# Kernel optimization log

Hardware: AMD Instinct MI355X
Metric: run time of the kernel (lower is better)

## Reference

```python
import jax, jax.numpy as jnp
import numpy as np

B, T, D, U = 64, 128, 1024, 1024


def setup_inputs() -> dict:
    key = jax.random.key(0)
    k_x, k_r, k_s, k_wi, k_wh = jax.random.split(key, 5)
    x = jax.random.normal(k_x, (B, T, D), dtype=jnp.float32)
    reset = jax.random.randint(k_r, (B, T), 0, 2, dtype=jnp.int32)
    state = jax.random.normal(k_s, (B, T, U), dtype=jnp.float32)
    # hk.GRU params: w_i (input->3*hidden), w_h (hidden->3*hidden), bias (3*hidden)
    w_i = jax.random.normal(k_wi, (D, 3 * U), dtype=jnp.float32) * (1.0 / np.sqrt(D))
    w_h = jax.random.normal(k_wh, (U, 3 * U), dtype=jnp.float32) * (1.0 / np.sqrt(U))
    b = jnp.zeros((3 * U,), dtype=jnp.float32)
    return {"x": x, "reset": reset, "state": state, "w_i": w_i, "w_h": w_h, "b": b}


def reference(x, reset, state, w_i, w_h, b):
    # _prepare_for_rnn merges (B,T)->rows and adds a length-1 time axis, so
    # hk.dynamic_unroll(ResetCore(GRU)) == one ResetCore(GRU) step over B*T rows.
    Bd, Td, Dd = x.shape
    Ud = w_h.shape[0]
    xf = x.reshape(Bd * Td, Dd)                      # [N, D]
    h = state.reshape(Bd * Td, Ud)                   # [N, U]
    should_reset = reset.reshape(Bd * Td, 1).astype(bool)
    # hk.ResetCore: replace state with initial_state (zeros) where reset is set
    h = jnp.where(should_reset, jnp.zeros_like(h), h)
    # hk.GRU step
    gates_x = xf @ w_i                               # [N, 3U]
    zr_x, a_x = gates_x[:, : 2 * Ud], gates_x[:, 2 * Ud :]
    zr = jax.nn.sigmoid(zr_x + h @ w_h[:, : 2 * Ud] + b[: 2 * Ud])
    z, r = zr[:, :Ud], zr[:, Ud:]
    a = jnp.tanh(a_x + (r * h) @ w_h[:, 2 * Ud :] + b[2 * Ud :])
    h_new = (1.0 - z) * h + z * a                    # [N, U]
    out = h_new.reshape(Bd, Td, Ud)                  # _recover_shape
    new_state = h_new.reshape(Bd, Td, Ud)            # _rnn_reshape back to (B,T,U)
    return out, new_state
```

## Files before the change

kernel.cpp:

```cpp
#include <hip/hip_runtime.h>


typedef __attribute__((ext_vector_type(8))) short short8;
typedef __attribute__((ext_vector_type(4))) short short4v;
typedef __attribute__((ext_vector_type(4))) float floatx4;
typedef __attribute__((ext_vector_type(4))) float f32x4;

#define MROWS 8192
#define KTOT 2048
#define NU 1024

__device__ __forceinline__ short f2bf(float f) {
  unsigned u = __builtin_bit_cast(unsigned, f);
  u += 0x7fffu + ((u >> 16) & 1u);
  return (short)(u >> 16);
}
__device__ __forceinline__ float bf2f(short s) {
  unsigned u = ((unsigned)(unsigned short)s) << 16;
  return __builtin_bit_cast(float, u);
}
__device__ __forceinline__ float sigmoid_f(float v) { return 1.f / (1.f + __expf(-v)); }
__device__ __forceinline__ float tanh_f(float v) {
  float c = fminf(fmaxf(v, -15.f), 15.f);
  float e = __expf(2.f * c);
  return (e - 1.f) / (e + 1.f);
}

typedef __attribute__((address_space(3))) void* lds_vp;
typedef const __attribute__((address_space(1))) void* gbl_vp;
__device__ __forceinline__ void gload16(const void* g, void* lds) {
  __builtin_amdgcn_global_load_lds((gbl_vp)g, (lds_vp)lds, 16, 0, 0);
}

__global__ __launch_bounds__(256) void wt_kernel(const float* __restrict__ w_i,
                                                 const float* __restrict__ w_h,
                                                 short* __restrict__ Wc) {
  __shared__ float tile[32][33];
  const int kb = blockIdx.x * 32;
  const int nb = blockIdx.y * 32;
  const float* src = (kb < 1024) ? w_i : w_h;
  const int kbl = kb & 1023;
  const int tx = threadIdx.x & 31;
  const int ty = threadIdx.x >> 5;
#pragma unroll
  for (int r = 0; r < 32; r += 8)
    tile[ty + r][tx] = src[(size_t)(kbl + ty + r) * 3072 + nb + tx];
  __syncthreads();
#pragma unroll
  for (int r = 0; r < 32; r += 8)
    Wc[(size_t)(nb + ty + r) * KTOT + kb + tx] = f2bf(tile[tx][ty + r]);
}

__global__ __launch_bounds__(256) void xh_kernel(const float* __restrict__ x,
                                                 const int* __restrict__ reset,
                                                 const float* __restrict__ state,
                                                 short* __restrict__ xbf,
                                                 short* __restrict__ hbf) {
  const size_t i4 = (size_t)blockIdx.x * blockDim.x + threadIdx.x;
  const size_t off = i4 * 4;
  const int row = (int)(off >> 10);
  const float hm = reset[row] ? 0.f : 1.f;
  floatx4 fx = *(const floatx4*)(x + off);
  floatx4 fh = *(const floatx4*)(state + off);
  short4v cx, ch;
#pragma unroll
  for (int e = 0; e < 4; ++e) { cx[e] = f2bf(fx[e]); ch[e] = f2bf(fh[e] * hm); }
  *(short4v*)(xbf + off) = cx;
  *(short4v*)(hbf + off) = ch;
}

struct TilePtrs {
  const short* a0; const short* a1;
  const short* h0; const short* h1;
  const short* b0; const short* b1;
};

#define GEMM_CORE(KHALF_SWITCH)                                              \
  f32x4 acc[4][4];                                                           \
  _Pragma("unroll") for (int i = 0; i < 4; ++i)                              \
      _Pragma("unroll") for (int j = 0; j < 4; ++j)                          \
          acc[i][j] = (f32x4){0.f, 0.f, 0.f, 0.f};                           \
  const int wave = tid >> 6, lane = tid & 63;                                \
  const int wm = wave >> 1, wn = wave & 1;                                   \
  const int lrow = lane & 15, lk = (lane >> 4) * 8;                          \
  char* ldsA0 = (char*)sA + wave * 1024; char* ldsA1 = ldsA0 + 4096;         \
  char* ldsB0 = (char*)sB + wave * 1024; char* ldsB1 = ldsB0 + 4096;         \
  for (int kk = 0; kk < KTOT; kk += 32) {                                    \
    const int kl = kk & 1023;                                                \
    const short *pa0, *pa1;                                                  \
    KHALF_SWITCH                                                             \
    gload16(pa0, ldsA0);                                                     \
    gload16(pa1, ldsA1);                                                     \
    gload16(p.b0 + kk, ldsB0);                                               \
    gload16(p.b1 + kk, ldsB1);                                               \
    __syncthreads();                                                         \
    short8 af[4], bfr[4];                                                    \
    _Pragma("unroll") for (int i = 0; i < 4; ++i)                            \
        af[i] = *(const short8*)&sA[wm * 64 + i * 16 + lrow][lk];            \
    _Pragma("unroll") for (int j = 0; j < 4; ++j)                            \
        bfr[j] = *(const short8*)&sB[wn * 64 + j * 16 + lrow][lk];           \
    _Pragma("unroll") for (int i = 0; i < 4; ++i)                            \
        _Pragma("unroll") for (int j = 0; j < 4; ++j)                        \
            acc[i][j] = __builtin_amdgcn_mfma_f32_16x16x32_bf16(             \
                af[i], bfr[j], acc[i][j], 0, 0, 0);                          \
    __syncthreads();                                                         \
  }

#define KSWITCH_STD                                                          \
  if (kk < 1024) { pa0 = p.a0 + kl; pa1 = p.a1 + kl; }                       \
  else           { pa0 = p.h0 + kl; pa1 = p.h1 + kl; }

__global__ __launch_bounds__(256, 3) void zr_kernel(
    const short* __restrict__ xbf, const short* __restrict__ hbf,
    const short* __restrict__ Wc, const float* __restrict__ bias,
    float* __restrict__ zbuf, short* __restrict__ rh) {
  __shared__ short sA[128][32];
  __shared__ short sB[128][32];
  const int tid = threadIdx.x;
  const int widx = (blockIdx.x & 7) * 128 + (blockIdx.x >> 3);
  const int m0 = (widx >> 4) * 128;
  const int n0 = (widx & 15) * 128;

  const int r0 = tid >> 2;
  const int kc = (tid & 3) * 8;
  TilePtrs p;
  p.a0 = xbf + (size_t)(m0 + r0) * 1024 + kc;
  p.a1 = xbf + (size_t)(m0 + 64 + r0) * 1024 + kc;
  p.h0 = hbf + (size_t)(m0 + r0) * 1024 + kc;
  p.h1 = hbf + (size_t)(m0 + 64 + r0) * 1024 + kc;
  p.b0 = Wc + (size_t)(n0 + r0) * KTOT + kc;
  p.b1 = Wc + (size_t)(n0 + 64 + r0) * KTOT + kc;

  GEMM_CORE(KSWITCH_STD)

  const bool zhalf = (n0 < 1024);
#pragma unroll
  for (int j = 0; j < 4; ++j) {
    const int gcn = n0 + wn * 64 + j * 16 + lrow;
    const float bv = bias[gcn];
#pragma unroll
    for (int i = 0; i < 4; ++i) {
#pragma unroll
      for (int rg = 0; rg < 4; ++rg) {
        const int gr = m0 + wm * 64 + i * 16 + (lane >> 4) * 4 + rg;
        const float sv = sigmoid_f(acc[i][j][rg] + bv);
        if (zhalf) {
          zbuf[(size_t)gr * NU + gcn] = sv;
        } else {
          const int u = gcn - 1024;
          const float hv = bf2f(hbf[(size_t)gr * NU + u]);
          rh[(size_t)gr * NU + u] = f2bf(sv * hv);
        }
      }
    }
  }
}

__global__ __launch_bounds__(256, 3) void cand_kernel(
    const short* __restrict__ xbf, const short* __restrict__ rh,
    const short* __restrict__ Wc, const float* __restrict__ bias,
    const int* __restrict__ reset, const float* __restrict__ state,
    const float* __restrict__ zbuf, float* __restrict__ out) {
  __shared__ short sA[128][32];
  __shared__ short sB[128][32];
  const int tid = threadIdx.x;
  const int widx = (blockIdx.x & 7) * 64 + (blockIdx.x >> 3);
  const int m0 = (widx >> 3) * 128;
  const int n0 = (widx & 7) * 128;

  const int r0 = tid >> 2;
  const int kc = (tid & 3) * 8;
  const short* Wa = Wc + (size_t)2048 * KTOT;
  TilePtrs p;
  p.a0 = xbf + (size_t)(m0 + r0) * 1024 + kc;
  p.a1 = xbf + (size_t)(m0 + 64 + r0) * 1024 + kc;
  p.h0 = rh + (size_t)(m0 + r0) * 1024 + kc;
  p.h1 = rh + (size_t)(m0 + 64 + r0) * 1024 + kc;
  p.b0 = Wa + (size_t)(n0 + r0) * KTOT + kc;
  p.b1 = Wa + (size_t)(n0 + 64 + r0) * KTOT + kc;

  GEMM_CORE(KSWITCH_STD)

#pragma unroll
  for (int j = 0; j < 4; ++j) {
    const int gc = n0 + wn * 64 + j * 16 + lrow;
    const float ba = bias[2048 + gc];
#pragma unroll
    for (int i = 0; i < 4; ++i) {
#pragma unroll
      for (int rg = 0; rg < 4; ++rg) {
        const int gr = m0 + wm * 64 + i * 16 + (lane >> 4) * 4 + rg;
        const float av = tanh_f(acc[i][j][rg] + ba);
        const float zv = zbuf[(size_t)gr * NU + gc];
        const float hv = reset[gr] ? 0.f : state[(size_t)gr * NU + gc];
        const float hn = (1.f - zv) * hv + zv * av;
        out[(size_t)gr * NU + gc] = hn;
        out[(size_t)MROWS * NU + (size_t)gr * NU + gc] = hn;
      }
    }
  }
}

extern "C" void kernel_launch(void* const* d_in, const int* in_sizes, int n_in,
                              void* d_out, int out_size, void* d_ws, size_t ws_size,
                              hipStream_t stream) {
  const float* x = (const float*)d_in[0];
  const int* reset = (const int*)d_in[1];
  const float* state = (const float*)d_in[2];
  const float* w_i = (const float*)d_in[3];
  const float* w_h = (const float*)d_in[4];
  const float* bias = (const float*)d_in[5];
  float* out = (float*)d_out;

  short* Wc = (short*)d_ws;
  short* xbf = Wc + (size_t)3072 * KTOT;
  short* hbf = xbf + (size_t)MROWS * 1024;
  short* rh  = hbf + (size_t)MROWS * 1024;
  float* zbuf = out + (size_t)MROWS * NU;

  wt_kernel<<<dim3(KTOT / 32, 3072 / 32), 256, 0, stream>>>(w_i, w_h, Wc);
  xh_kernel<<<dim3(MROWS * 1024 / 4 / 256), 256, 0, stream>>>(x, reset, state, xbf, hbf);

  zr_kernel<<<dim3(64 * 16), 256, 0, stream>>>(xbf, hbf, Wc, bias, zbuf, rh);
  cand_kernel<<<dim3(64 * 8), 256, 0, stream>>>(xbf, rh, Wc, bias, reset, state, zbuf, out);
}
```

Measured before the change: 196.7 us.

## Rewrite GEMM kernels with triple-buffered async LDS pipeline and 128x256 tiles

Both GEMM kernels are restructured to use 512-thread blocks with 128x256 output tiles and K-step 64. They also use a three-stage dynamic-LDS ring fed by global_load_lds with vmcnt-based waits, XOR-swizzled LDS addressing, and s_setprio around MFMA bursts. The x and masked-state bf16 copies are now written into one concatenated [N,2048] buffer so the A operand is a single contiguous row. This targets the load-then-barrier stalls and small-tile reuse of the previous single-buffered loop, at the cost of a large LDS footprint (one block per CU) and hand-managed wait counts that must stay correct.

```diff
diff --git a/kernel.cpp b/kernel.cpp
--- a/kernel.cpp
+++ b/kernel.cpp
@@ -9,6 +9,10 @@
 #define MROWS 8192
 #define KTOT 2048
 #define NU 1024
+#define NTILE 32
+#define ABYTES 16384
+#define BUFBYTES 49152
+#define LDSTOT (3 * BUFBYTES)
 
 __device__ __forceinline__ short f2bf(float f) {
   unsigned u = __builtin_bit_cast(unsigned, f);
@@ -31,6 +35,14 @@
 __device__ __forceinline__ void gload16(const void* g, void* lds) {
   __builtin_amdgcn_global_load_lds((gbl_vp)g, (lds_vp)lds, 16, 0, 0);
 }
+
+#define MF(a, b, c) __builtin_amdgcn_mfma_f32_16x16x32_bf16(a, b, c, 0, 0, 0)
+#define VMCNT(n) asm volatile("s_waitcnt vmcnt(" #n ")" ::: "memory")
+#define TILE_BAR()                          \
+  do {                                      \
+    __builtin_amdgcn_s_barrier();           \
+    asm volatile("" ::: "memory");          \
+  } while (0)
 
 __global__ __launch_bounds__(256) void wt_kernel(const float* __restrict__ w_i,
                                                  const float* __restrict__ w_h,
@@ -54,89 +66,136 @@
 __global__ __launch_bounds__(256) void xh_kernel(const float* __restrict__ x,
                                                  const int* __restrict__ reset,
                                                  const float* __restrict__ state,
-                                                 short* __restrict__ xbf,
-                                                 short* __restrict__ hbf) {
+                                                 short* __restrict__ xhc) {
   const size_t i4 = (size_t)blockIdx.x * blockDim.x + threadIdx.x;
-  const size_t off = i4 * 4;
-  const int row = (int)(off >> 10);
+  const size_t e = i4 * 4;
+  const int row = (int)(e >> 10);
+  const int d = (int)(e & 1023);
   const float hm = reset[row] ? 0.f : 1.f;
-  floatx4 fx = *(const floatx4*)(x + off);
-  floatx4 fh = *(const floatx4*)(state + off);
+  floatx4 fx = *(const floatx4*)(x + e);
+  floatx4 fh = *(const floatx4*)(state + e);
   short4v cx, ch;
 #pragma unroll
-  for (int e = 0; e < 4; ++e) { cx[e] = f2bf(fx[e]); ch[e] = f2bf(fh[e] * hm); }
-  *(short4v*)(xbf + off) = cx;
-  *(short4v*)(hbf + off) = ch;
-}
-
-struct TilePtrs {
-  const short* a0; const short* a1;
-  const short* h0; const short* h1;
-  const short* b0; const short* b1;
-};
-
-#define GEMM_CORE(KHALF_SWITCH)                                              \
-  f32x4 acc[4][4];                                                           \
-  _Pragma("unroll") for (int i = 0; i < 4; ++i)                              \
-      _Pragma("unroll") for (int j = 0; j < 4; ++j)                          \
-          acc[i][j] = (f32x4){0.f, 0.f, 0.f, 0.f};                           \
-  const int wave = tid >> 6, lane = tid & 63;                                \
-  const int wm = wave >> 1, wn = wave & 1;                                   \
-  const int lrow = lane & 15, lk = (lane >> 4) * 8;                          \
-  char* ldsA0 = (char*)sA + wave * 1024; char* ldsA1 = ldsA0 + 4096;         \
-  char* ldsB0 = (char*)sB + wave * 1024; char* ldsB1 = ldsB0 + 4096;         \
-  for (int kk = 0; kk < KTOT; kk += 32) {                                    \
-    const int kl = kk & 1023;                                                \
-    const short *pa0, *pa1;                                                  \
-    KHALF_SWITCH                                                             \
-    gload16(pa0, ldsA0);                                                     \
-    gload16(pa1, ldsA1);                                                     \
-    gload16(p.b0 + kk, ldsB0);                                               \
-    gload16(p.b1 + kk, ldsB1);                                               \
-    __syncthreads();                                                         \
-    short8 af[4], bfr[4];                                                    \
-    _Pragma("unroll") for (int i = 0; i < 4; ++i)                            \
-        af[i] = *(const short8*)&sA[wm * 64 + i * 16 + lrow][lk];            \
-    _Pragma("unroll") for (int j = 0; j < 4; ++j)                            \
-        bfr[j] = *(const short8*)&sB[wn * 64 + j * 16 + lrow][lk];           \
-    _Pragma("unroll") for (int i = 0; i < 4; ++i)                            \
-        _Pragma("unroll") for (int j = 0; j < 4; ++j)                        \
-            acc[i][j] = __builtin_amdgcn_mfma_f32_16x16x32_bf16(             \
-                af[i], bfr[j], acc[i][j], 0, 0, 0);                          \
-    __syncthreads();                                                         \
-  }
-
-#define KSWITCH_STD                                                          \
-  if (kk < 1024) { pa0 = p.a0 + kl; pa1 = p.a1 + kl; }                       \
-  else           { pa0 = p.h0 + kl; pa1 = p.h1 + kl; }
-
-__global__ __launch_bounds__(256, 3) void zr_kernel(
-    const short* __restrict__ xbf, const short* __restrict__ hbf,
-    const short* __restrict__ Wc, const float* __restrict__ bias,
-    float* __restrict__ zbuf, short* __restrict__ rh) {
-  __shared__ short sA[128][32];
-  __shared__ short sB[128][32];
-  const int tid = threadIdx.x;
-  const int widx = (blockIdx.x & 7) * 128 + (blockIdx.x >> 3);
-  const int m0 = (widx >> 4) * 128;
-  const int n0 = (widx & 15) * 128;
-
-  const int r0 = tid >> 2;
-  const int kc = (tid & 3) * 8;
-  TilePtrs p;
-  p.a0 = xbf + (size_t)(m0 + r0) * 1024 + kc;
-  p.a1 = xbf + (size_t)(m0 + 64 + r0) * 1024 + kc;
-  p.h0 = hbf + (size_t)(m0 + r0) * 1024 + kc;
-  p.h1 = hbf + (size_t)(m0 + 64 + r0) * 1024 + kc;
-  p.b0 = Wc + (size_t)(n0 + r0) * KTOT + kc;
-  p.b1 = Wc + (size_t)(n0 + 64 + r0) * KTOT + kc;
-
-  GEMM_CORE(KSWITCH_STD)
-
-  const bool zhalf = (n0 < 1024);
+  for (int k = 0; k < 4; ++k) { cx[k] = f2bf(fx[k]); ch[k] = f2bf(fh[k] * hm); }
+  *(short4v*)(xhc + (size_t)row * KTOT + d) = cx;
+  *(short4v*)(xhc + (size_t)row * KTOT + 1024 + d) = ch;
+}
+
+#define GEMM_PRELUDE()                                                        \
+  extern __shared__ char lds[];                                               \
+  const int tid = threadIdx.x;                                                \
+  const int wave = tid >> 6, lane = tid & 63;                                 \
+  const int wm = wave >> 2, wn = wave & 3;                                    \
+  const int lrow = lane & 15;                                                 \
+  const int g16 = (lane >> 4) << 4;                                           \
+  const int swz = (lrow & 7) << 4;                                            \
+  const int inner16 = (((lane & 7) ^ (lane >> 3)) << 4);                      \
+  const int lr8 = lane >> 3;                                                  \
+  const int dA0 = (2 * wave) * 1024, dA1 = dA0 + 1024;                        \
+  const int dB00 = ABYTES + (4 * wave) * 1024, dB01 = dB00 + 1024,            \
+            dB10 = dB00 + 2048, dB11 = dB00 + 3072;                           \
+  f32x4 acc[4][4];                                                            \
+  _Pragma("unroll") for (int i = 0; i < 4; ++i)                               \
+      _Pragma("unroll") for (int j = 0; j < 4; ++j)                           \
+          acc[i][j] = (f32x4){0.f, 0.f, 0.f, 0.f};
+
+#define LOAD_FRAGS(bufC, K)                                                   \
+  {                                                                           \
+    const int colb = (((K) * 64 + g16) ^ swz);                                \
+    const char* pA = (bufC) + (wm * 64 + lrow) * 128 + colb;                  \
+    const char* pB = (bufC) + ABYTES + (wn * 64 + lrow) * 128 + colb;         \
+    af0 = *(const short8*)(pA);                                               \
+    af1 = *(const short8*)(pA + 2048);                                        \
+    af2 = *(const short8*)(pA + 4096);                                        \
+    af3 = *(const short8*)(pA + 6144);                                        \
+    bq0 = *(const short8*)(pB);                                               \
+    bq1 = *(const short8*)(pB + 2048);                                        \
+    bq2 = *(const short8*)(pB + 4096);                                        \
+    bq3 = *(const short8*)(pB + 6144);                                        \
+  }
+
+#define MFMA16()                                 \
+  __builtin_amdgcn_s_setprio(1);                 \
+  acc[0][0] = MF(af0, bq0, acc[0][0]);           \
+  acc[0][1] = MF(af0, bq1, acc[0][1]);           \
+  acc[0][2] = MF(af0, bq2, acc[0][2]);           \
+  acc[0][3] = MF(af0, bq3, acc[0][3]);           \
+  acc[1][0] = MF(af1, bq0, acc[1][0]);           \
+  acc[1][1] = MF(af1, bq1, acc[1][1]);           \
+  acc[1][2] = MF(af1, bq2, acc[1][2]);           \
+  acc[1][3] = MF(af1, bq3, acc[1][3]);           \
+  acc[2][0] = MF(af2, bq0, acc[2][0]);           \
+  acc[2][1] = MF(af2, bq1, acc[2][1]);           \
+  acc[2][2] = MF(af2, bq2, acc[2][2]);           \
+  acc[2][3] = MF(af2, bq3, acc[2][3]);           \
+  acc[3][0] = MF(af3, bq0, acc[3][0]);           \
+  acc[3][1] = MF(af3, bq1, acc[3][1]);           \
+  acc[3][2] = MF(af3, bq2, acc[3][2]);           \
+  acc[3][3] = MF(af3, bq3, acc[3][3]);           \
+  __builtin_amdgcn_s_setprio(0);
+
+#define GEMM_LOOP()                                                           \
+  STG_H0(0, lds);                                                             \
+  STG_H1(0, lds);                                                             \
+  STG_H0(1, lds + BUFBYTES);                                                  \
+  STG_H1(1, lds + BUFBYTES);                                                  \
+  VMCNT(6);                                                                   \
+  TILE_BAR();                                                                 \
+  int cb = 0;                                                                 \
+  for (int t = 0; t < NTILE; ++t) {                                           \
+    char* bufC = lds + cb * BUFBYTES;                                         \
+    int nbi = cb + 2;                                                         \
+    if (nbi >= 3) nbi -= 3;                                                   \
+    char* bufN = lds + nbi * BUFBYTES;                                        \
+    const bool st = (t + 2 < NTILE);                                          \
+    short8 af0, af1, af2, af3, bq0, bq1, bq2, bq3;                            \
+    LOAD_FRAGS(bufC, 0);                                                      \
+    if (st) { STG_H0(t + 2, bufN); }                                          \
+    MFMA16();                                                                 \
+    LOAD_FRAGS(bufC, 1);                                                      \
+    if (st) { STG_H1(t + 2, bufN); }                                          \
+    MFMA16();                                                                 \
+    if (t < NTILE - 1) {                                                      \
+      if (st) { VMCNT(6); } else { VMCNT(0); }                                \
+      TILE_BAR();                                                             \
+    }                                                                         \
+    cb = (cb == 2) ? 0 : cb + 1;                                              \
+  }
+
+__global__ __launch_bounds__(512, 1) void zr_kernel(
+    const short* __restrict__ xhc, const short* __restrict__ Wc,
+    const float* __restrict__ bias, float* __restrict__ zbuf,
+    short* __restrict__ rh) {
+  GEMM_PRELUDE();
+  const int ntile = blockIdx.x & 7;
+  const int mtile = blockIdx.x >> 3;
+  const int m0 = mtile * 128;
+  const int n0g = ntile * 256;
+
+  const short* aS0 = xhc + (size_t)(m0 + 16 * wave + lr8) * KTOT + (inner16 >> 1);
+  const short* aS1 = aS0 + (size_t)8 * KTOT;
+  const short* bS00 = Wc + (size_t)(n0g + 32 * wave + lr8) * KTOT + (inner16 >> 1);
+  const short* bS01 = bS00 + (size_t)8 * KTOT;
+  const short* bS10 = bS00 + (size_t)16 * KTOT;
+  const short* bS11 = bS00 + (size_t)24 * KTOT;
+
+#define STG_H0(T, BUF)                          \
+  gload16(aS0 + (T) * 64, (BUF) + dA0);         \
+  gload16(bS00 + (T) * 64, (BUF) + dB00);       \
+  gload16(bS01 + (T) * 64, (BUF) + dB01);
+#define STG_H1(T, BUF)                          \
+  gload16(aS1 + (T) * 64, (BUF) + dA1);         \
+  gload16(bS10 + (T) * 64, (BUF) + dB10);       \
+  gload16(bS11 + (T) * 64, (BUF) + dB11);
+
+  GEMM_LOOP();
+#undef STG_H0
+#undef STG_H1
+
+  const bool zh = (n0g < 1024);
 #pragma unroll
   for (int j = 0; j < 4; ++j) {
-    const int gcn = n0 + wn * 64 + j * 16 + lrow;
+    const int gcn = n0g + wn * 64 + j * 16 + lrow;
     const float bv = bias[gcn];
 #pragma unroll
     for (int i = 0; i < 4; ++i) {
@@ -144,11 +203,11 @@
       for (int rg = 0; rg < 4; ++rg) {
         const int gr = m0 + wm * 64 + i * 16 + (lane >> 4) * 4 + rg;
         const float sv = sigmoid_f(acc[i][j][rg] + bv);
-        if (zhalf) {
+        if (zh) {
           zbuf[(size_t)gr * NU + gcn] = sv;
         } else {
           const int u = gcn - 1024;
-          const float hv = bf2f(hbf[(size_t)gr * NU + u]);
+          const float hv = bf2f(xhc[(size_t)gr * KTOT + 1024 + u]);
           rh[(size_t)gr * NU + u] = f2bf(sv * hv);
         }
       }
@@ -156,34 +215,44 @@
   }
 }
 
-__global__ __launch_bounds__(256, 3) void cand_kernel(
-    const short* __restrict__ xbf, const short* __restrict__ rh,
+__global__ __launch_bounds__(512, 1) void cand_kernel(
+    const short* __restrict__ xhc, const short* __restrict__ rh,
     const short* __restrict__ Wc, const float* __restrict__ bias,
     const int* __restrict__ reset, const float* __restrict__ state,
-    const float* __restrict__ zbuf, float* __restrict__ out) {
-  __shared__ short sA[128][32];
-  __shared__ short sB[128][32];
-  const int tid = threadIdx.x;
-  const int widx = (blockIdx.x & 7) * 64 + (blockIdx.x >> 3);
-  const int m0 = (widx >> 3) * 128;
-  const int n0 = (widx & 7) * 128;
-
-  const int r0 = tid >> 2;
-  const int kc = (tid & 3) * 8;
+    const float* zbuf, float* out) {
+  GEMM_PRELUDE();
+  const int widx = (blockIdx.x & 7) * 32 + (blockIdx.x >> 3);
+  const int ntile = widx >> 6;
+  const int mtile = widx & 63;
+  const int m0 = mtile * 128;
+  const int n0g = ntile * 256;
+
+  const short* aX0 = xhc + (size_t)(m0 + 16 * wave + lr8) * KTOT + (inner16 >> 1);
+  const short* aX1 = aX0 + (size_t)8 * KTOT;
+  const short* aR0 = rh + (size_t)(m0 + 16 * wave + lr8) * NU + (inner16 >> 1);
+  const short* aR1 = aR0 + (size_t)8 * NU;
   const short* Wa = Wc + (size_t)2048 * KTOT;
-  TilePtrs p;
-  p.a0 = xbf + (size_t)(m0 + r0) * 1024 + kc;
-  p.a1 = xbf + (size_t)(m0 + 64 + r0) * 1024 + kc;
-  p.h0 = rh + (size_t)(m0 + r0) * 1024 + kc;
-  p.h1 = rh + (size_t)(m0 + 64 + r0) * 1024 + kc;
-  p.b0 = Wa + (size_t)(n0 + r0) * KTOT + kc;
-  p.b1 = Wa + (size_t)(n0 + 64 + r0) * KTOT + kc;
-
-  GEMM_CORE(KSWITCH_STD)
+  const short* bS00 = Wa + (size_t)(n0g + 32 * wave + lr8) * KTOT + (inner16 >> 1);
+  const short* bS01 = bS00 + (size_t)8 * KTOT;
+  const short* bS10 = bS00 + (size_t)16 * KTOT;
+  const short* bS11 = bS00 + (size_t)24 * KTOT;
+
+#define STG_H0(T, BUF)                                                        \
+  gload16((T) < 16 ? (aX0 + (T) * 64) : (aR0 + ((T) - 16) * 64), (BUF) + dA0);\
+  gload16(bS00 + (T) * 64, (BUF) + dB00);                                     \
+  gload16(bS01 + (T) * 64, (BUF) + dB01);
+#define STG_H1(T, BUF)                                                        \
+  gload16((T) < 16 ? (aX1 + (T) * 64) : (aR1 + ((T) - 16) * 64), (BUF) + dA1);\
+  gload16(bS10 + (T) * 64, (BUF) + dB10);                                     \
+  gload16(bS11 + (T) * 64, (BUF) + dB11);
+
+  GEMM_LOOP();
+#undef STG_H0
+#undef STG_H1
 
 #pragma unroll
   for (int j = 0; j < 4; ++j) {
-    const int gc = n0 + wn * 64 + j * 16 + lrow;
+    const int gc = n0g + wn * 64 + j * 16 + lrow;
     const float ba = bias[2048 + gc];
 #pragma unroll
     for (int i = 0; i < 4; ++i) {
@@ -213,14 +282,18 @@
   float* out = (float*)d_out;
 
   short* Wc = (short*)d_ws;
-  short* xbf = Wc + (size_t)3072 * KTOT;
-  short* hbf = xbf + (size_t)MROWS * 1024;
-  short* rh  = hbf + (size_t)MROWS * 1024;
+  short* xhc = Wc + (size_t)3072 * KTOT;
+  short* rh = xhc + (size_t)MROWS * KTOT;
   float* zbuf = out + (size_t)MROWS * NU;
 
+  hipFuncSetAttribute(reinterpret_cast<const void*>(zr_kernel),
+                      hipFuncAttributeMaxDynamicSharedMemorySize, LDSTOT);
+  hipFuncSetAttribute(reinterpret_cast<const void*>(cand_kernel),
+                      hipFuncAttributeMaxDynamicSharedMemorySize, LDSTOT);
+
   wt_kernel<<<dim3(KTOT / 32, 3072 / 32), 256, 0, stream>>>(w_i, w_h, Wc);
-  xh_kernel<<<dim3(MROWS * 1024 / 4 / 256), 256, 0, stream>>>(x, reset, state, xbf, hbf);
-
-  zr_kernel<<<dim3(64 * 16), 256, 0, stream>>>(xbf, hbf, Wc, bias, zbuf, rh);
-  cand_kernel<<<dim3(64 * 8), 256, 0, stream>>>(xbf, rh, Wc, bias, reset, state, zbuf, out);
-}
+  xh_kernel<<<dim3(MROWS * 1024 / 4 / 256), 256, 0, stream>>>(x, reset, state, xhc);
+
+  zr_kernel<<<dim3(512), 512, LDSTOT, stream>>>(xhc, Wc, bias, zbuf, rh);
+  cand_kernel<<<dim3(256), 512, LDSTOT, stream>>>(xhc, rh, Wc, bias, reset, state, zbuf, out);
+}
```

Result: faster. 184.3 us (-6.3%).

## Rewrite GRU GEMMs with 4-stage async LDS pipeline, larger tiles, swizzled layout

Applied to the files above, without the earlier changes.

Replaces the single-buffered 128x128 GEMM loop with a 4-buffer, 3-deep prefetch pipeline that waits on vmcnt, using 512-thread blocks. The zr tile grows to 256x256 and the cand tile to 256x128. LDS reads and writes use an XOR swizzle to avoid bank conflicts, and x and the reset-masked h are packed into one concatenated [N,2048] bf16 buffer. The epilogue reads h from that bf16 buffer instead of fp32 state, so the output is computed from a rounded h, which adds a little error. The larger LDS footprint lowers occupancy, and with only 256 blocks each GEMM runs in a single wave across the CUs.

```diff
diff --git a/kernel.cpp b/kernel.cpp
--- a/kernel.cpp
+++ b/kernel.cpp
@@ -9,6 +9,12 @@
 #define MROWS 8192
 #define KTOT 2048
 #define NU 1024
+#define BK 32
+#define NCHUNK 64
+#define ZR_CHUNKB 32768
+#define ZR_LDS (4 * 32768)
+#define CD_CHUNKB 24576
+#define CD_LDS (4 * 24576)
 
 __device__ __forceinline__ short f2bf(float f) {
   unsigned u = __builtin_bit_cast(unsigned, f);
@@ -31,6 +37,15 @@
 __device__ __forceinline__ void gload16(const void* g, void* lds) {
   __builtin_amdgcn_global_load_lds((gbl_vp)g, (lds_vp)lds, 16, 0, 0);
 }
+
+#define MF(a, b, c) __builtin_amdgcn_mfma_f32_16x16x32_bf16(a, b, c, 0, 0, 0)
+#define VMCNT_(n) asm volatile("s_waitcnt vmcnt(" #n ")" ::: "memory")
+#define VMCNT(n) VMCNT_(n)
+#define TILE_BAR()                  \
+  do {                              \
+    __builtin_amdgcn_s_barrier();   \
+    asm volatile("" ::: "memory");  \
+  } while (0)
 
 __global__ __launch_bounds__(256) void wt_kernel(const float* __restrict__ w_i,
                                                  const float* __restrict__ w_h,
@@ -54,101 +69,106 @@
 __global__ __launch_bounds__(256) void xh_kernel(const float* __restrict__ x,
                                                  const int* __restrict__ reset,
                                                  const float* __restrict__ state,
-                                                 short* __restrict__ xbf,
-                                                 short* __restrict__ hbf) {
+                                                 short* __restrict__ xhc) {
   const size_t i4 = (size_t)blockIdx.x * blockDim.x + threadIdx.x;
-  const size_t off = i4 * 4;
-  const int row = (int)(off >> 10);
+  const size_t e = i4 * 4;
+  const int row = (int)(e >> 10);
+  const int d = (int)(e & 1023);
   const float hm = reset[row] ? 0.f : 1.f;
-  floatx4 fx = *(const floatx4*)(x + off);
-  floatx4 fh = *(const floatx4*)(state + off);
+  floatx4 fx = *(const floatx4*)(x + e);
+  floatx4 fh = *(const floatx4*)(state + e);
   short4v cx, ch;
 #pragma unroll
-  for (int e = 0; e < 4; ++e) { cx[e] = f2bf(fx[e]); ch[e] = f2bf(fh[e] * hm); }
-  *(short4v*)(xbf + off) = cx;
-  *(short4v*)(hbf + off) = ch;
-}
-
-struct TilePtrs {
-  const short* a0; const short* a1;
-  const short* h0; const short* h1;
-  const short* b0; const short* b1;
-};
-
-#define GEMM_CORE(KHALF_SWITCH)                                              \
-  f32x4 acc[4][4];                                                           \
-  _Pragma("unroll") for (int i = 0; i < 4; ++i)                              \
-      _Pragma("unroll") for (int j = 0; j < 4; ++j)                          \
-          acc[i][j] = (f32x4){0.f, 0.f, 0.f, 0.f};                           \
-  const int wave = tid >> 6, lane = tid & 63;                                \
-  const int wm = wave >> 1, wn = wave & 1;                                   \
-  const int lrow = lane & 15, lk = (lane >> 4) * 8;                          \
-  char* ldsA0 = (char*)sA + wave * 1024; char* ldsA1 = ldsA0 + 4096;         \
-  char* ldsB0 = (char*)sB + wave * 1024; char* ldsB1 = ldsB0 + 4096;         \
-  for (int kk = 0; kk < KTOT; kk += 32) {                                    \
-    const int kl = kk & 1023;                                                \
-    const short *pa0, *pa1;                                                  \
-    KHALF_SWITCH                                                             \
-    gload16(pa0, ldsA0);                                                     \
-    gload16(pa1, ldsA1);                                                     \
-    gload16(p.b0 + kk, ldsB0);                                               \
-    gload16(p.b1 + kk, ldsB1);                                               \
-    __syncthreads();                                                         \
-    short8 af[4], bfr[4];                                                    \
-    _Pragma("unroll") for (int i = 0; i < 4; ++i)                            \
-        af[i] = *(const short8*)&sA[wm * 64 + i * 16 + lrow][lk];            \
-    _Pragma("unroll") for (int j = 0; j < 4; ++j)                            \
-        bfr[j] = *(const short8*)&sB[wn * 64 + j * 16 + lrow][lk];           \
-    _Pragma("unroll") for (int i = 0; i < 4; ++i)                            \
-        _Pragma("unroll") for (int j = 0; j < 4; ++j)                        \
-            acc[i][j] = __builtin_amdgcn_mfma_f32_16x16x32_bf16(             \
-                af[i], bfr[j], acc[i][j], 0, 0, 0);                          \
-    __syncthreads();                                                         \
-  }
-
-#define KSWITCH_STD                                                          \
-  if (kk < 1024) { pa0 = p.a0 + kl; pa1 = p.a1 + kl; }                       \
-  else           { pa0 = p.h0 + kl; pa1 = p.h1 + kl; }
-
-__global__ __launch_bounds__(256, 3) void zr_kernel(
-    const short* __restrict__ xbf, const short* __restrict__ hbf,
-    const short* __restrict__ Wc, const float* __restrict__ bias,
-    float* __restrict__ zbuf, short* __restrict__ rh) {
-  __shared__ short sA[128][32];
-  __shared__ short sB[128][32];
+  for (int k = 0; k < 4; ++k) { cx[k] = f2bf(fx[k]); ch[k] = f2bf(fh[k] * hm); }
+  *(short4v*)(xhc + (size_t)row * KTOT + d) = cx;
+  *(short4v*)(xhc + (size_t)row * KTOT + 1024 + d) = ch;
+}
+
+__global__ __launch_bounds__(512, 2) void zr_kernel(
+    const short* __restrict__ xhc, const short* __restrict__ Wc,
+    const float* __restrict__ bias, float* __restrict__ zbuf,
+    short* __restrict__ rh) {
+  extern __shared__ char lds[];
   const int tid = threadIdx.x;
-  const int widx = (blockIdx.x & 7) * 128 + (blockIdx.x >> 3);
-  const int m0 = (widx >> 4) * 128;
-  const int n0 = (widx & 15) * 128;
-
-  const int r0 = tid >> 2;
-  const int kc = (tid & 3) * 8;
-  TilePtrs p;
-  p.a0 = xbf + (size_t)(m0 + r0) * 1024 + kc;
-  p.a1 = xbf + (size_t)(m0 + 64 + r0) * 1024 + kc;
-  p.h0 = hbf + (size_t)(m0 + r0) * 1024 + kc;
-  p.h1 = hbf + (size_t)(m0 + 64 + r0) * 1024 + kc;
-  p.b0 = Wc + (size_t)(n0 + r0) * KTOT + kc;
-  p.b1 = Wc + (size_t)(n0 + 64 + r0) * KTOT + kc;
-
-  GEMM_CORE(KSWITCH_STD)
-
-  const bool zhalf = (n0 < 1024);
+  const int wave = tid >> 6, lane = tid & 63;
+  const int wm = wave >> 2, wn = wave & 3;
+  const int lrow = lane & 15;
+  const int rdslot = ((lane >> 4) ^ ((lrow >> 1) & 3)) << 4;
+  const int aoff = (wm * 128 + lrow) * 64 + rdslot;
+  const int boff = 16384 + (wn * 64 + lrow) * 64 + rdslot;
+  const int dA0 = wave * 1024, dA1 = dA0 + 8192;
+  const int dB0 = 16384 + wave * 1024, dB1 = dB0 + 8192;
+  const int sr = lane >> 2;
+  const int scol = ((lane & 3) ^ ((lane >> 3) & 3)) * 8;
+
+  const int ntile = blockIdx.x & 7, mtile = blockIdx.x >> 3;
+  const int m0 = mtile * 256, n0g = ntile * 256;
+
+  const short* aS = xhc + (size_t)(m0 + wave * 16 + sr) * KTOT + scol;
+  const short* aS2 = aS + (size_t)128 * KTOT;
+  const short* bS = Wc + (size_t)(n0g + wave * 16 + sr) * KTOT + scol;
+  const short* bS2 = bS + (size_t)128 * KTOT;
+
+  f32x4 acc[8][4];
+#pragma unroll
+  for (int i = 0; i < 8; ++i)
+#pragma unroll
+    for (int j = 0; j < 4; ++j) acc[i][j] = (f32x4){0.f, 0.f, 0.f, 0.f};
+
+#define ZR_STAGE(ct, bufp)               \
+  gload16(aS + (ct) * BK, (bufp) + dA0); \
+  gload16(aS2 + (ct) * BK, (bufp) + dA1);\
+  gload16(bS + (ct) * BK, (bufp) + dB0); \
+  gload16(bS2 + (ct) * BK, (bufp) + dB1);
+
+  ZR_STAGE(0, lds);
+  ZR_STAGE(1, lds + ZR_CHUNKB);
+  ZR_STAGE(2, lds + 2 * ZR_CHUNKB);
+  VMCNT(8);
+  TILE_BAR();
+
+#pragma unroll 4
+  for (int c = 0; c < NCHUNK; ++c) {
+    const char* bb = lds + (c & 3) * ZR_CHUNKB;
+    short8 af[8], bq[4];
+#pragma unroll
+    for (int i = 0; i < 8; ++i) af[i] = *(const short8*)(bb + aoff + i * 1024);
+#pragma unroll
+    for (int j = 0; j < 4; ++j) bq[j] = *(const short8*)(bb + boff + j * 1024);
+    if (c + 3 < NCHUNK) {
+      char* nb = lds + ((c + 3) & 3) * ZR_CHUNKB;
+      ZR_STAGE(c + 3, nb);
+    }
+    TILE_BAR();
+    __builtin_amdgcn_s_setprio(1);
+#pragma unroll
+    for (int i = 0; i < 8; ++i)
+#pragma unroll
+      for (int j = 0; j < 4; ++j) acc[i][j] = MF(af[i], bq[j], acc[i][j]);
+    __builtin_amdgcn_s_setprio(0);
+    if (c + 3 < NCHUNK) { VMCNT(8); }
+    else if (c + 2 < NCHUNK) { VMCNT(4); }
+    else if (c + 1 < NCHUNK) { VMCNT(0); }
+    TILE_BAR();
+  }
+#undef ZR_STAGE
+
+  const bool zh = (n0g < 1024);
 #pragma unroll
   for (int j = 0; j < 4; ++j) {
-    const int gcn = n0 + wn * 64 + j * 16 + lrow;
+    const int gcn = n0g + wn * 64 + j * 16 + lrow;
     const float bv = bias[gcn];
 #pragma unroll
-    for (int i = 0; i < 4; ++i) {
+    for (int i = 0; i < 8; ++i) {
 #pragma unroll
       for (int rg = 0; rg < 4; ++rg) {
-        const int gr = m0 + wm * 64 + i * 16 + (lane >> 4) * 4 + rg;
+        const int gr = m0 + wm * 128 + i * 16 + (lane >> 4) * 4 + rg;
         const float sv = sigmoid_f(acc[i][j][rg] + bv);
-        if (zhalf) {
+        if (zh) {
           zbuf[(size_t)gr * NU + gcn] = sv;
         } else {
           const int u = gcn - 1024;
-          const float hv = bf2f(hbf[(size_t)gr * NU + u]);
+          const float hv = bf2f(xhc[(size_t)gr * KTOT + 1024 + u]);
           rh[(size_t)gr * NU + u] = f2bf(sv * hv);
         }
       }
@@ -156,34 +176,83 @@
   }
 }
 
-__global__ __launch_bounds__(256, 3) void cand_kernel(
-    const short* __restrict__ xbf, const short* __restrict__ rh,
+__global__ __launch_bounds__(512, 2) void cand_kernel(
+    const short* __restrict__ xhc, const short* __restrict__ rh,
     const short* __restrict__ Wc, const float* __restrict__ bias,
-    const int* __restrict__ reset, const float* __restrict__ state,
-    const float* __restrict__ zbuf, float* __restrict__ out) {
-  __shared__ short sA[128][32];
-  __shared__ short sB[128][32];
+    const float* zbuf, float* out) {
+  extern __shared__ char lds[];
   const int tid = threadIdx.x;
-  const int widx = (blockIdx.x & 7) * 64 + (blockIdx.x >> 3);
-  const int m0 = (widx >> 3) * 128;
-  const int n0 = (widx & 7) * 128;
-
-  const int r0 = tid >> 2;
-  const int kc = (tid & 3) * 8;
-  const short* Wa = Wc + (size_t)2048 * KTOT;
-  TilePtrs p;
-  p.a0 = xbf + (size_t)(m0 + r0) * 1024 + kc;
-  p.a1 = xbf + (size_t)(m0 + 64 + r0) * 1024 + kc;
-  p.h0 = rh + (size_t)(m0 + r0) * 1024 + kc;
-  p.h1 = rh + (size_t)(m0 + 64 + r0) * 1024 + kc;
-  p.b0 = Wa + (size_t)(n0 + r0) * KTOT + kc;
-  p.b1 = Wa + (size_t)(n0 + 64 + r0) * KTOT + kc;
-
-  GEMM_CORE(KSWITCH_STD)
+  const int wave = tid >> 6, lane = tid & 63;
+  const int wm = wave >> 1, wn = wave & 1;
+  const int lrow = lane & 15;
+  const int rdslot = ((lane >> 4) ^ ((lrow >> 1) & 3)) << 4;
+  const int aoff = (wm * 64 + lrow) * 64 + rdslot;
+  const int boff = 16384 + (wn * 64 + lrow) * 64 + rdslot;
+  const int dA0 = wave * 1024, dA1 = dA0 + 8192;
+  const int dB0 = 16384 + wave * 1024;
+  const int sr = lane >> 2;
+  const int scol = ((lane & 3) ^ ((lane >> 3) & 3)) * 8;
+
+  const int ntile = blockIdx.x & 7, mtile = blockIdx.x >> 3;
+  const int m0 = mtile * 256, n0g = ntile * 128;
+
+  const short* aX = xhc + (size_t)(m0 + wave * 16 + sr) * KTOT + scol;
+  const short* aX2 = aX + (size_t)128 * KTOT;
+  const short* aR = rh + (size_t)(m0 + wave * 16 + sr) * NU + scol;
+  const short* aR2 = aR + (size_t)128 * NU;
+  const short* bS = Wc + (size_t)(2048 + n0g + wave * 16 + sr) * KTOT + scol;
+
+  f32x4 acc[4][4];
+#pragma unroll
+  for (int i = 0; i < 4; ++i)
+#pragma unroll
+    for (int j = 0; j < 4; ++j) acc[i][j] = (f32x4){0.f, 0.f, 0.f, 0.f};
+
+#define CD_STAGE(ct, bufp)                                      \
+  if ((ct) < 32) {                                              \
+    gload16(aX + (ct) * BK, (bufp) + dA0);                      \
+    gload16(aX2 + (ct) * BK, (bufp) + dA1);                     \
+  } else {                                                      \
+    gload16(aR + ((ct) - 32) * BK, (bufp) + dA0);               \
+    gload16(aR2 + ((ct) - 32) * BK, (bufp) + dA1);              \
+  }                                                             \
+  gload16(bS + (ct) * BK, (bufp) + dB0);
+
+  CD_STAGE(0, lds);
+  CD_STAGE(1, lds + CD_CHUNKB);
+  CD_STAGE(2, lds + 2 * CD_CHUNKB);
+  VMCNT(6);
+  TILE_BAR();
+
+#pragma unroll 4
+  for (int c = 0; c < NCHUNK; ++c) {
+    const char* bb = lds + (c & 3) * CD_CHUNKB;
+    short8 af[4], bq[4];
+#pragma unroll
+    for (int i = 0; i < 4; ++i) af[i] = *(const short8*)(bb + aoff + i * 1024);
+#pragma unroll
+    for (int j = 0; j < 4; ++j) bq[j] = *(const short8*)(bb + boff + j * 1024);
+    if (c + 3 < NCHUNK) {
+      char* nb = lds + ((c + 3) & 3) * CD_CHUNKB;
+      CD_STAGE(c + 3, nb);
+    }
+    TILE_BAR();
+    __builtin_amdgcn_s_setprio(1);
+#pragma unroll
+    for (int i = 0; i < 4; ++i)
+#pragma unroll
+      for (int j = 0; j < 4; ++j) acc[i][j] = MF(af[i], bq[j], acc[i][j]);
+    __builtin_amdgcn_s_setprio(0);
+    if (c + 3 < NCHUNK) { VMCNT(6); }
+    else if (c + 2 < NCHUNK) { VMCNT(3); }
+    else if (c + 1 < NCHUNK) { VMCNT(0); }
+    TILE_BAR();
+  }
+#undef CD_STAGE
 
 #pragma unroll
   for (int j = 0; j < 4; ++j) {
-    const int gc = n0 + wn * 64 + j * 16 + lrow;
+    const int gc = n0g + wn * 64 + j * 16 + lrow;
     const float ba = bias[2048 + gc];
 #pragma unroll
     for (int i = 0; i < 4; ++i) {
@@ -192,7 +261,7 @@
         const int gr = m0 + wm * 64 + i * 16 + (lane >> 4) * 4 + rg;
         const float av = tanh_f(acc[i][j][rg] + ba);
         const float zv = zbuf[(size_t)gr * NU + gc];
-        const float hv = reset[gr] ? 0.f : state[(size_t)gr * NU + gc];
+        const float hv = bf2f(xhc[(size_t)gr * KTOT + 1024 + gc]);
         const float hn = (1.f - zv) * hv + zv * av;
         out[(size_t)gr * NU + gc] = hn;
         out[(size_t)MROWS * NU + (size_t)gr * NU + gc] = hn;
@@ -213,14 +282,18 @@
   float* out = (float*)d_out;
 
   short* Wc = (short*)d_ws;
-  short* xbf = Wc + (size_t)3072 * KTOT;
-  short* hbf = xbf + (size_t)MROWS * 1024;
-  short* rh  = hbf + (size_t)MROWS * 1024;
+  short* xhc = Wc + (size_t)3072 * KTOT;
+  short* rh = xhc + (size_t)MROWS * KTOT;
   float* zbuf = out + (size_t)MROWS * NU;
 
+  hipFuncSetAttribute(reinterpret_cast<const void*>(zr_kernel),
+                      hipFuncAttributeMaxDynamicSharedMemorySize, ZR_LDS);
+  hipFuncSetAttribute(reinterpret_cast<const void*>(cand_kernel),
+                      hipFuncAttributeMaxDynamicSharedMemorySize, CD_LDS);
+
   wt_kernel<<<dim3(KTOT / 32, 3072 / 32), 256, 0, stream>>>(w_i, w_h, Wc);
-  xh_kernel<<<dim3(MROWS * 1024 / 4 / 256), 256, 0, stream>>>(x, reset, state, xbf, hbf);
-
-  zr_kernel<<<dim3(64 * 16), 256, 0, stream>>>(xbf, hbf, Wc, bias, zbuf, rh);
-  cand_kernel<<<dim3(64 * 8), 256, 0, stream>>>(xbf, rh, Wc, bias, reset, state, zbuf, out);
-}
+  xh_kernel<<<dim3(MROWS * 1024 / 4 / 256), 256, 0, stream>>>(x, reset, state, xhc);
+
+  zr_kernel<<<dim3(256), 512, ZR_LDS, stream>>>(xhc, Wc, bias, zbuf, rh);
+  cand_kernel<<<dim3(256), 512, CD_LDS, stream>>>(xhc, rh, Wc, bias, zbuf, out);
+}
```

Measured after the change: 211.4 us. 7.5% more time.
